# Optimization experiments

Hardware: AMD Instinct MI355X
Metric: run time of the kernel (lower is better)

The kernel has to match this reference:

```python
import jax, jax.numpy as jnp
import numpy as np

LR = 0.01
WD = 0.01


def _lfltm(params, x):
    w1, b1, w2, b2 = params
    return jnp.tanh(x @ w1 + b1) @ w2 + b2  # [N, D]


def _deep_opt_elem(Wm1, bm1, Wm2, bm2, g):
    # per-parameter-element learned optimizer: scalar grad -> hidden(M) -> scalar update
    h = jnp.tanh(g[..., None] * Wm1 + bm1)  # [..., M]
    return h @ Wm2 + bm2[0]


def setup_inputs() -> dict:
    key = jax.random.key(0)
    ks = jax.random.split(key, 8)
    N, D, H, M = 16384, 512, 1024, 32
    return {
        "x_t": jax.random.normal(ks[0], (N, D), jnp.float32),
        "x_target": jax.random.normal(ks[1], (N, D), jnp.float32),
        "w1": jax.random.normal(ks[2], (D, H), jnp.float32) * 0.02,
        "b1": jnp.zeros((H,), jnp.float32),
        "w2": jax.random.normal(ks[3], (H, D), jnp.float32) * 0.02,
        "b2": jnp.zeros((D,), jnp.float32),
        "Wm1": jax.random.normal(ks[4], (M,), jnp.float32) * 0.1,
        "bm1": jnp.zeros((M,), jnp.float32),
        "Wm2": jax.random.normal(ks[5], (M,), jnp.float32) * 0.1,
        "bm2": jnp.zeros((1,), jnp.float32),
    }


def reference(x_t, x_target, w1, b1, w2, b2, Wm1, bm1, Wm2, bm2):
    mem = (w1, b1, w2, b2)

    # retrieve: h_t = LFLTM(memory_state, x_t)
    h_t = _lfltm(mem, x_t)

    # analytic per-step gradient of MSE loss through the memory MLP
    def compute_loss(params):
        pred = _lfltm(params, x_t)
        return jnp.mean((pred - x_target) ** 2)

    grads = jax.grad(compute_loss)(mem)

    # learned optimizer on each gradient tensor, then fast-weight update
    new_mem = tuple(
        p - (LR * _deep_opt_elem(Wm1, bm1, Wm2, bm2, g) + WD * p)
        for p, g in zip(mem, grads)
    )

    return (h_t,) + new_mem
```

## Files before the change

### kernel.cpp

```cpp
#include <hip/hip_runtime.h>
#include <hip/hip_bf16.h>

#define LR 0.01f
#define WD 0.01f
#define NTHREADS 256

typedef short s16x8 __attribute__((ext_vector_type(8)));
typedef float f32x4 __attribute__((ext_vector_type(4)));
typedef unsigned short u16;

__device__ __forceinline__ u16 f2bf(float f) {
    __hip_bfloat16 h = __float2bfloat16(f);
    return *reinterpret_cast<u16*>(&h);
}
__device__ __forceinline__ float bf2f(u16 u) {
    __hip_bfloat16 h;
    *reinterpret_cast<u16*>(&h) = u;
    return __bfloat162float(h);
}
__device__ __forceinline__ float tanh_fast(float x) {
    float t = fminf(fmaxf(2.f * x, -30.f), 30.f);
    float e = __expf(t);
    return 1.f - 2.f * __builtin_amdgcn_rcpf(e + 1.f);
}

__device__ __forceinline__ void stage_pair(const u16* gA, const u16* gB, int ldg,
                                           u16* lds) {
    const int t = threadIdx.x;
#pragma unroll
    for (int q = 0; q < 4; ++q) {
        int s = t + q * 256;
        int row = s >> 3, chp = s & 7;
        int chl = chp ^ (row & 7);
        const u16* gp = (chl < 4) ? (gA + (size_t)row * ldg + chl * 8)
                                  : (gB + (size_t)row * ldg + (chl & 3) * 8);
        __builtin_amdgcn_global_load_lds(
            (const __attribute__((address_space(1))) void*)gp,
            (__attribute__((address_space(3))) void*)(lds + s * 8), 16, 0, 0);
    }
}

__device__ __forceinline__ s16x8 frag(const u16* P, int r, int c) {
    return *(const s16x8*)(P + r * 64 + ((c ^ (r & 7)) * 8));
}

template <int NPROD, int EPI>
__global__ __launch_bounds__(NTHREADS) void k_mfma(
    const u16* __restrict__ Ah, const u16* __restrict__ Al,
    const u16* __restrict__ Bh, const u16* __restrict__ Bl,
    int nbx, int Md, int Nd, int Kd, int Kslice,
    const float* __restrict__ bias, const float* __restrict__ xtgt,
    const u16* __restrict__ Th,
    float* __restrict__ outf, u16* __restrict__ outb, u16* __restrict__ outbT,
    float scale) {
    constexpr int PAIRS = (NPROD > 1) ? 2 : 1;
    __shared__ u16 smem[2 * PAIRS * 8192];

    const int nwg = gridDim.x;
    const int sw = (blockIdx.x & 7) * (nwg >> 3) + (blockIdx.x >> 3);
    const int m0 = (sw / nbx) * 128, n0 = (sw % nbx) * 128;
    const int kb = blockIdx.y * Kslice;

    const int lane = threadIdx.x & 63, wid = threadIdx.x >> 6;
    const int wrow = (wid >> 1) * 64, wcol = (wid & 1) * 64;
    const int lm = lane & 15;
    const int cA = lane >> 4;

    f32x4 acc[4][4] = {};

    const u16* gAh = Ah + (size_t)m0 * Kd + kb;
    const u16* gBh = Bh + (size_t)n0 * Kd + kb;
    const u16* gAl = (NPROD == 3) ? Al + (size_t)m0 * Kd + kb : nullptr;
    const u16* gBl = (NPROD >= 2) ? Bl + (size_t)n0 * Kd + kb : nullptr;

    auto stage_all = [&](int buf, int ko) {
        u16* base = smem + buf * (PAIRS * 8192);
        stage_pair(gAh + ko, gBh + ko, Kd, base);
        if (NPROD == 3) stage_pair(gAl + ko, gBl + ko, Kd, base + 8192);
        if (NPROD == 2) stage_pair(gBl + ko, gBl + ko, Kd, base + 8192);
    };

    stage_all(0, 0);
    __syncthreads();

    int cur = 0;
    for (int k0 = 0; k0 < Kslice; k0 += 32, cur ^= 1) {
        if (k0 + 32 < Kslice) stage_all(cur ^ 1, k0 + 32);
        const u16* P1 = smem + cur * (PAIRS * 8192);
        const u16* P2 = P1 + 8192;
        s16x8 ah[4], bh[4], al[4], bl[4];
#pragma unroll
        for (int i = 0; i < 4; ++i) {
            ah[i] = frag(P1, wrow + i * 16 + lm, cA);
            bh[i] = frag(P1, wcol + i * 16 + lm, cA + 4);
            if (NPROD == 3) {
                al[i] = frag(P2, wrow + i * 16 + lm, cA);
                bl[i] = frag(P2, wcol + i * 16 + lm, cA + 4);
            }
            if (NPROD == 2) bl[i] = frag(P2, wcol + i * 16 + lm, cA);
        }
#pragma unroll
        for (int i = 0; i < 4; ++i)
#pragma unroll
            for (int j = 0; j < 4; ++j) {
                acc[i][j] = __builtin_amdgcn_mfma_f32_16x16x32_bf16(
                    ah[i], bh[j], acc[i][j], 0, 0, 0);
                if (NPROD >= 2)
                    acc[i][j] = __builtin_amdgcn_mfma_f32_16x16x32_bf16(
                        ah[i], bl[j], acc[i][j], 0, 0, 0);
                if (NPROD == 3)
                    acc[i][j] = __builtin_amdgcn_mfma_f32_16x16x32_bf16(
                        al[i], bh[j], acc[i][j], 0, 0, 0);
            }
        __syncthreads();
    }

    const int rbase = (lane >> 4) * 4;
#pragma unroll
    for (int i = 0; i < 4; ++i) {
        const int row0 = m0 + wrow + i * 16 + rbase;
#pragma unroll
        for (int j = 0; j < 4; ++j) {
            const int col = n0 + wcol + j * 16 + lm;
            if (EPI == 0) {
                ushort4 hv;
                float b = bias[col];
                hv.x = f2bf(tanh_fast(acc[i][j][0] + b));
                hv.y = f2bf(tanh_fast(acc[i][j][1] + b));
                hv.z = f2bf(tanh_fast(acc[i][j][2] + b));
                hv.w = f2bf(tanh_fast(acc[i][j][3] + b));
                outb[(size_t)(row0 + 0) * Nd + col] = hv.x;
                outb[(size_t)(row0 + 1) * Nd + col] = hv.y;
                outb[(size_t)(row0 + 2) * Nd + col] = hv.z;
                outb[(size_t)(row0 + 3) * Nd + col] = hv.w;
                *(ushort4*)(outbT + (size_t)col * Md + row0) = hv;
            } else if (EPI == 1) {
                ushort4 gv;
#pragma unroll
                for (int r = 0; r < 4; ++r) {
                    size_t idx = (size_t)(row0 + r) * Nd + col;
                    float p = acc[i][j][r] + bias[col];
                    outf[idx] = p;
                    u16 g = f2bf(scale * (p - xtgt[idx]));
                    outb[idx] = g;
                    ((u16*)&gv)[r] = g;
                }
                *(ushort4*)(outbT + (size_t)col * Md + row0) = gv;
            } else if (EPI == 2) {
                ushort4 dv;
#pragma unroll
                for (int r = 0; r < 4; ++r) {
                    size_t idx = (size_t)(row0 + r) * Nd + col;
                    float tv = bf2f(Th[idx]);
                    ((u16*)&dv)[r] = f2bf(acc[i][j][r] * (1.0f - tv * tv));
                }
                *(ushort4*)(outbT + (size_t)col * Md + row0) = dv;
            } else {
#pragma unroll
                for (int r = 0; r < 4; ++r)
                    atomicAdd(&outf[(size_t)(row0 + r) * Nd + col], acc[i][j][r]);
            }
        }
    }
}

__global__ void k_prep(const float* __restrict__ in, u16* __restrict__ hiRM,
                       u16* __restrict__ loRM, u16* __restrict__ hiT,
                       u16* __restrict__ loT, int R, int C) {
    __shared__ float tile[64][65];
    const int tx = threadIdx.x & 63, ty = threadIdx.x >> 6;
    const int c0 = blockIdx.x * 64, r0 = blockIdx.y * 64;
#pragma unroll
    for (int i = 0; i < 64; i += 4) {
        size_t idx = (size_t)(r0 + ty + i) * C + c0 + tx;
        float v = in[idx];
        tile[ty + i][tx] = v;
        if (hiRM) {
            u16 h = f2bf(v);
            hiRM[idx] = h;
            if (loRM) loRM[idx] = f2bf(v - bf2f(h));
        }
    }
    __syncthreads();
    if (hiT) {
#pragma unroll
        for (int i = 0; i < 64; i += 4) {
            float v = tile[tx][ty + i];
            u16 h = f2bf(v);
            size_t o = (size_t)(c0 + ty + i) * R + r0 + tx;
            hiT[o] = h;
            if (loT) loT[o] = f2bf(v - bf2f(h));
        }
    }
}

__global__ void k_rowsum(const u16* __restrict__ src, float* __restrict__ dst,
                         int C) {
    const int row = blockIdx.x * 4 + (threadIdx.x >> 6);
    const int lane = threadIdx.x & 63;
    const u16* p = src + (size_t)row * C;
    float s = 0.f;
    for (int c = lane * 8; c < C; c += 64 * 8) {
        s16x8 v = *(const s16x8*)(p + c);
#pragma unroll
        for (int e = 0; e < 8; ++e) s += bf2f((u16)v[e]);
    }
#pragma unroll
    for (int off = 32; off; off >>= 1) s += __shfl_down(s, off);
    if (lane == 0) dst[row] = s;
}

__global__ void k_update(const float* __restrict__ p, const float* __restrict__ g,
                         float* __restrict__ out, int n,
                         const float* __restrict__ Wm1, const float* __restrict__ bm1,
                         const float* __restrict__ Wm2, const float* __restrict__ bm2,
                         int M) {
    __shared__ float s1[64], s2[64], s3[64];
    if (threadIdx.x < M) {
        s1[threadIdx.x] = Wm1[threadIdx.x];
        s2[threadIdx.x] = bm1[threadIdx.x];
        s3[threadIdx.x] = Wm2[threadIdx.x];
    }
    __syncthreads();
    int i = blockIdx.x * blockDim.x + threadIdx.x;
    if (i >= n) return;
    float gv = g[i];
    float u = bm2[0];
#pragma unroll 8
    for (int m = 0; m < M; ++m) u += tanh_fast(fmaf(gv, s1[m], s2[m])) * s3[m];
    float pv = p[i];
    out[i] = pv - (LR * u + WD * pv);
}

__global__ void k_zero(float* __restrict__ p, int n) {
    int i = blockIdx.x * blockDim.x + threadIdx.x;
    if (i < n) p[i] = 0.f;
}

extern "C" void kernel_launch(void* const* d_in, const int* in_sizes, int n_in,
                              void* d_out, int out_size, void* d_ws, size_t ws_size,
                              hipStream_t stream) {
    const float* x_t      = (const float*)d_in[0];
    const float* x_target = (const float*)d_in[1];
    const float* w1  = (const float*)d_in[2];
    const float* b1  = (const float*)d_in[3];
    const float* w2  = (const float*)d_in[4];
    const float* b2  = (const float*)d_in[5];
    const float* Wm1 = (const float*)d_in[6];
    const float* bm1 = (const float*)d_in[7];
    const float* Wm2 = (const float*)d_in[8];
    const float* bm2 = (const float*)d_in[9];

    const int H = in_sizes[3];
    const int D = in_sizes[5];
    const int N = in_sizes[0] / D;
    const int M = in_sizes[6];

    char* w = (char*)d_ws;
    float* gw2 = (float*)w;            w += (size_t)H * D * 4;
    float* gw1 = (float*)w;            w += (size_t)D * H * 4;
    float* gb1 = (float*)w;            w += (size_t)H * 4;
    float* gb2 = (float*)w;            w += (size_t)D * 4;
    u16* T_hi = (u16*)w;               w += (size_t)N * H * 2;
    u16* TT   = (u16*)w;               w += (size_t)N * H * 2;
    u16* dAT  = (u16*)w;               w += (size_t)N * H * 2;
    u16* Gb   = (u16*)w;               w += (size_t)N * D * 2;
    u16* x_hi = (u16*)w;               w += (size_t)N * D * 2;
    u16* x_lo = (u16*)w;               w += (size_t)N * D * 2;
    u16* xT   = (u16*)w;               w += (size_t)N * D * 2;
    u16* w1T_hi = (u16*)w;             w += (size_t)D * H * 2;
    u16* w1T_lo = (u16*)w;             w += (size_t)D * H * 2;
    u16* w2T_hi = (u16*)w;             w += (size_t)D * H * 2;
    u16* w2T_lo = (u16*)w;             w += (size_t)D * H * 2;
    u16* w2b_hi = (u16*)w;             w += (size_t)H * D * 2;
    u16* GT = x_lo;

    float* out  = (float*)d_out;
    float* h_t  = out;
    float* o_w1 = h_t + (size_t)N * D;
    float* o_b1 = o_w1 + (size_t)D * H;
    float* o_w2 = o_b1 + H;
    float* o_b2 = o_w2 + (size_t)H * D;

    dim3 blk(NTHREADS);
    const float scale = 2.0f / ((float)N * (float)D);

    int zn = H * D + D * H;
    k_zero<<<dim3((zn + NTHREADS - 1) / NTHREADS), blk, 0, stream>>>(gw2, zn);

    k_prep<<<dim3(D / 64, N / 64), blk, 0, stream>>>(x_t, x_hi, x_lo, xT, nullptr, N, D);
    k_prep<<<dim3(H / 64, D / 64), blk, 0, stream>>>(w1, nullptr, nullptr, w1T_hi, w1T_lo, D, H);
    k_prep<<<dim3(D / 64, H / 64), blk, 0, stream>>>(w2, w2b_hi, nullptr, w2T_hi, w2T_lo, H, D);

    k_mfma<3, 0><<<dim3((H / 128) * (N / 128), 1), blk, 0, stream>>>(
        x_hi, x_lo, w1T_hi, w1T_lo, H / 128, N, H, D, D, b1, nullptr, nullptr,
        nullptr, T_hi, TT, 0.f);

    k_mfma<2, 1><<<dim3((D / 128) * (N / 128), 1), blk, 0, stream>>>(
        T_hi, nullptr, w2T_hi, w2T_lo, D / 128, N, D, H, H, b2, x_target, nullptr,
        h_t, Gb, GT, scale);

    k_mfma<1, 2><<<dim3((H / 128) * (N / 128), 1), blk, 0, stream>>>(
        Gb, nullptr, w2b_hi, nullptr, H / 128, N, H, D, D, nullptr, nullptr, T_hi,
        nullptr, nullptr, dAT, 0.f);

    const int SPLIT = 16;
    k_mfma<1, 3><<<dim3((D / 128) * (H / 128), SPLIT), blk, 0, stream>>>(
        TT, nullptr, GT, nullptr, D / 128, H, D, N, N / SPLIT, nullptr, nullptr,
        nullptr, gw2, nullptr, nullptr, 0.f);

    k_mfma<1, 3><<<dim3((H / 128) * (D / 128), SPLIT), blk, 0, stream>>>(
        xT, nullptr, dAT, nullptr, H / 128, D, H, N, N / SPLIT, nullptr, nullptr,
        nullptr, gw1, nullptr, nullptr, 0.f);

    k_rowsum<<<dim3(H / 4), blk, 0, stream>>>(dAT, gb1, N);
    k_rowsum<<<dim3(D / 4), blk, 0, stream>>>(GT, gb2, N);

    k_update<<<dim3((D * H + NTHREADS - 1) / NTHREADS), blk, 0, stream>>>(
        w1, gw1, o_w1, D * H, Wm1, bm1, Wm2, bm2, M);
    k_update<<<dim3((H + NTHREADS - 1) / NTHREADS), blk, 0, stream>>>(
        b1, gb1, o_b1, H, Wm1, bm1, Wm2, bm2, M);
    k_update<<<dim3((H * D + NTHREADS - 1) / NTHREADS), blk, 0, stream>>>(
        w2, gw2, o_w2, H * D, Wm1, bm1, Wm2, bm2, M);
    k_update<<<dim3((D + NTHREADS - 1) / NTHREADS), blk, 0, stream>>>(
        b2, gb2, o_b2, D, Wm1, bm1, Wm2, bm2, M);
}
```

Before: 440.2 us.

## Replace split-bf16 compensated GEMMs with single fp16 MFMA and scaled gradients

Drops the hi/lo bf16 split products (3 and 2 MFMAs per tile) and runs every GEMM as a single fp16 MFMA pass. To fit the small output gradient in fp16 range, it is pre-scaled by 2^20 and the scale is removed in the update kernel. This cuts the MFMA work, LDS staging and prep traffic for the forward GEMMs. The trade-off is reduced precision (fp16 mantissa, no compensation) and a risk of overflow or underflow in the scaled intermediates.

```diff
diff --git a/kernel.cpp b/kernel.cpp
--- a/kernel.cpp
+++ b/kernel.cpp
@@ -4,19 +4,22 @@
 #define LR 0.01f
 #define WD 0.01f
 #define NTHREADS 256
+#define SCALE_G 1048576.0f
+#define INV_SCALE_G 9.5367431640625e-07f
 
 typedef short s16x8 __attribute__((ext_vector_type(8)));
+typedef _Float16 f16x8 __attribute__((ext_vector_type(8)));
 typedef float f32x4 __attribute__((ext_vector_type(4)));
 typedef unsigned short u16;
 
-__device__ __forceinline__ u16 f2bf(float f) {
-    __hip_bfloat16 h = __float2bfloat16(f);
+__device__ __forceinline__ u16 f2h(float f) {
+    _Float16 h = (_Float16)f;
     return *reinterpret_cast<u16*>(&h);
 }
-__device__ __forceinline__ float bf2f(u16 u) {
-    __hip_bfloat16 h;
+__device__ __forceinline__ float h2f(u16 u) {
+    _Float16 h;
     *reinterpret_cast<u16*>(&h) = u;
-    return __bfloat162float(h);
+    return (float)h;
 }
 __device__ __forceinline__ float tanh_fast(float x) {
     float t = fminf(fmaxf(2.f * x, -30.f), 30.f);
@@ -40,21 +43,19 @@
     }
 }
 
-__device__ __forceinline__ s16x8 frag(const u16* P, int r, int c) {
-    return *(const s16x8*)(P + r * 64 + ((c ^ (r & 7)) * 8));
-}
-
-template <int NPROD, int EPI>
+__device__ __forceinline__ f16x8 frag(const u16* P, int r, int c) {
+    return *(const f16x8*)(P + r * 64 + ((c ^ (r & 7)) * 8));
+}
+
+template <int EPI>
 __global__ __launch_bounds__(NTHREADS) void k_mfma(
-    const u16* __restrict__ Ah, const u16* __restrict__ Al,
-    const u16* __restrict__ Bh, const u16* __restrict__ Bl,
+    const u16* __restrict__ A, const u16* __restrict__ Bt,
     int nbx, int Md, int Nd, int Kd, int Kslice,
     const float* __restrict__ bias, const float* __restrict__ xtgt,
     const u16* __restrict__ Th,
     float* __restrict__ outf, u16* __restrict__ outb, u16* __restrict__ outbT,
     float scale) {
-    constexpr int PAIRS = (NPROD > 1) ? 2 : 1;
-    __shared__ u16 smem[2 * PAIRS * 8192];
+    __shared__ u16 smem[2 * 8192];
 
     const int nwg = gridDim.x;
     const int sw = (blockIdx.x & 7) * (nwg >> 3) + (blockIdx.x >> 3);
@@ -68,50 +69,29 @@
 
     f32x4 acc[4][4] = {};
 
-    const u16* gAh = Ah + (size_t)m0 * Kd + kb;
-    const u16* gBh = Bh + (size_t)n0 * Kd + kb;
-    const u16* gAl = (NPROD == 3) ? Al + (size_t)m0 * Kd + kb : nullptr;
-    const u16* gBl = (NPROD >= 2) ? Bl + (size_t)n0 * Kd + kb : nullptr;
-
-    auto stage_all = [&](int buf, int ko) {
-        u16* base = smem + buf * (PAIRS * 8192);
-        stage_pair(gAh + ko, gBh + ko, Kd, base);
-        if (NPROD == 3) stage_pair(gAl + ko, gBl + ko, Kd, base + 8192);
-        if (NPROD == 2) stage_pair(gBl + ko, gBl + ko, Kd, base + 8192);
-    };
-
-    stage_all(0, 0);
+    const u16* gA = A + (size_t)m0 * Kd + kb;
+    const u16* gB = Bt + (size_t)n0 * Kd + kb;
+
+    stage_pair(gA, gB, Kd, smem);
     __syncthreads();
 
     int cur = 0;
     for (int k0 = 0; k0 < Kslice; k0 += 32, cur ^= 1) {
-        if (k0 + 32 < Kslice) stage_all(cur ^ 1, k0 + 32);
-        const u16* P1 = smem + cur * (PAIRS * 8192);
-        const u16* P2 = P1 + 8192;
-        s16x8 ah[4], bh[4], al[4], bl[4];
+        if (k0 + 32 < Kslice)
+            stage_pair(gA + k0 + 32, gB + k0 + 32, Kd, smem + (cur ^ 1) * 8192);
+        const u16* P1 = smem + cur * 8192;
+        f16x8 a[4], b[4];
 #pragma unroll
         for (int i = 0; i < 4; ++i) {
-            ah[i] = frag(P1, wrow + i * 16 + lm, cA);
-            bh[i] = frag(P1, wcol + i * 16 + lm, cA + 4);
-            if (NPROD == 3) {
-                al[i] = frag(P2, wrow + i * 16 + lm, cA);
-                bl[i] = frag(P2, wcol + i * 16 + lm, cA + 4);
-            }
-            if (NPROD == 2) bl[i] = frag(P2, wcol + i * 16 + lm, cA);
+            a[i] = frag(P1, wrow + i * 16 + lm, cA);
+            b[i] = frag(P1, wcol + i * 16 + lm, cA + 4);
         }
 #pragma unroll
         for (int i = 0; i < 4; ++i)
 #pragma unroll
-            for (int j = 0; j < 4; ++j) {
-                acc[i][j] = __builtin_amdgcn_mfma_f32_16x16x32_bf16(
-                    ah[i], bh[j], acc[i][j], 0, 0, 0);
-                if (NPROD >= 2)
-                    acc[i][j] = __builtin_amdgcn_mfma_f32_16x16x32_bf16(
-                        ah[i], bl[j], acc[i][j], 0, 0, 0);
-                if (NPROD == 3)
-                    acc[i][j] = __builtin_amdgcn_mfma_f32_16x16x32_bf16(
-                        al[i], bh[j], acc[i][j], 0, 0, 0);
-            }
+            for (int j = 0; j < 4; ++j)
+                acc[i][j] = __builtin_amdgcn_mfma_f32_16x16x32_f16(
+                    a[i], b[j], acc[i][j], 0, 0, 0);
         __syncthreads();
     }
 
@@ -124,11 +104,11 @@
             const int col = n0 + wcol + j * 16 + lm;
             if (EPI == 0) {
                 ushort4 hv;
-                float b = bias[col];
-                hv.x = f2bf(tanh_fast(acc[i][j][0] + b));
-                hv.y = f2bf(tanh_fast(acc[i][j][1] + b));
-                hv.z = f2bf(tanh_fast(acc[i][j][2] + b));
-                hv.w = f2bf(tanh_fast(acc[i][j][3] + b));
+                float bcol = bias[col];
+                hv.x = f2h(tanh_fast(acc[i][j][0] + bcol));
+                hv.y = f2h(tanh_fast(acc[i][j][1] + bcol));
+                hv.z = f2h(tanh_fast(acc[i][j][2] + bcol));
+                hv.w = f2h(tanh_fast(acc[i][j][3] + bcol));
                 outb[(size_t)(row0 + 0) * Nd + col] = hv.x;
                 outb[(size_t)(row0 + 1) * Nd + col] = hv.y;
                 outb[(size_t)(row0 + 2) * Nd + col] = hv.z;
@@ -141,7 +121,7 @@
                     size_t idx = (size_t)(row0 + r) * Nd + col;
                     float p = acc[i][j][r] + bias[col];
                     outf[idx] = p;
-                    u16 g = f2bf(scale * (p - xtgt[idx]));
+                    u16 g = f2h(scale * (p - xtgt[idx]));
                     outb[idx] = g;
                     ((u16*)&gv)[r] = g;
                 }
@@ -151,8 +131,8 @@
 #pragma unroll
                 for (int r = 0; r < 4; ++r) {
                     size_t idx = (size_t)(row0 + r) * Nd + col;
-                    float tv = bf2f(Th[idx]);
-                    ((u16*)&dv)[r] = f2bf(acc[i][j][r] * (1.0f - tv * tv));
+                    float tv = h2f(Th[idx]);
+                    ((u16*)&dv)[r] = f2h(acc[i][j][r] * (1.0f - tv * tv));
                 }
                 *(ushort4*)(outbT + (size_t)col * Md + row0) = dv;
             } else {
@@ -164,9 +144,8 @@
     }
 }
 
-__global__ void k_prep(const float* __restrict__ in, u16* __restrict__ hiRM,
-                       u16* __restrict__ loRM, u16* __restrict__ hiT,
-                       u16* __restrict__ loT, int R, int C) {
+__global__ void k_prep(const float* __restrict__ in, u16* __restrict__ rm,
+                       u16* __restrict__ tr, int R, int C) {
     __shared__ float tile[64][65];
     const int tx = threadIdx.x & 63, ty = threadIdx.x >> 6;
     const int c0 = blockIdx.x * 64, r0 = blockIdx.y * 64;
@@ -175,22 +154,13 @@
         size_t idx = (size_t)(r0 + ty + i) * C + c0 + tx;
         float v = in[idx];
         tile[ty + i][tx] = v;
-        if (hiRM) {
-            u16 h = f2bf(v);
-            hiRM[idx] = h;
-            if (loRM) loRM[idx] = f2bf(v - bf2f(h));
-        }
+        if (rm) rm[idx] = f2h(v);
     }
     __syncthreads();
-    if (hiT) {
-#pragma unroll
-        for (int i = 0; i < 64; i += 4) {
-            float v = tile[tx][ty + i];
-            u16 h = f2bf(v);
-            size_t o = (size_t)(c0 + ty + i) * R + r0 + tx;
-            hiT[o] = h;
-            if (loT) loT[o] = f2bf(v - bf2f(h));
-        }
+    if (tr) {
+#pragma unroll
+        for (int i = 0; i < 64; i += 4)
+            tr[(size_t)(c0 + ty + i) * R + r0 + tx] = f2h(tile[tx][ty + i]);
     }
 }
 
@@ -203,7 +173,7 @@
     for (int c = lane * 8; c < C; c += 64 * 8) {
         s16x8 v = *(const s16x8*)(p + c);
 #pragma unroll
-        for (int e = 0; e < 8; ++e) s += bf2f((u16)v[e]);
+        for (int e = 0; e < 8; ++e) s += h2f((u16)v[e]);
     }
 #pragma unroll
     for (int off = 32; off; off >>= 1) s += __shfl_down(s, off);
@@ -214,7 +184,7 @@
                          float* __restrict__ out, int n,
                          const float* __restrict__ Wm1, const float* __restrict__ bm1,
                          const float* __restrict__ Wm2, const float* __restrict__ bm2,
-                         int M) {
+                         int M, float invScale) {
     __shared__ float s1[64], s2[64], s3[64];
     if (threadIdx.x < M) {
         s1[threadIdx.x] = Wm1[threadIdx.x];
@@ -224,7 +194,7 @@
     __syncthreads();
     int i = blockIdx.x * blockDim.x + threadIdx.x;
     if (i >= n) return;
-    float gv = g[i];
+    float gv = g[i] * invScale;
     float u = bm2[0];
 #pragma unroll 8
     for (int m = 0; m < M; ++m) u += tanh_fast(fmaf(gv, s1[m], s2[m])) * s3[m];
@@ -261,19 +231,16 @@
     float* gw1 = (float*)w;            w += (size_t)D * H * 4;
     float* gb1 = (float*)w;            w += (size_t)H * 4;
     float* gb2 = (float*)w;            w += (size_t)D * 4;
-    u16* T_hi = (u16*)w;               w += (size_t)N * H * 2;
+    u16* Tf   = (u16*)w;               w += (size_t)N * H * 2;
     u16* TT   = (u16*)w;               w += (size_t)N * H * 2;
     u16* dAT  = (u16*)w;               w += (size_t)N * H * 2;
     u16* Gb   = (u16*)w;               w += (size_t)N * D * 2;
-    u16* x_hi = (u16*)w;               w += (size_t)N * D * 2;
-    u16* x_lo = (u16*)w;               w += (size_t)N * D * 2;
+    u16* GT   = (u16*)w;               w += (size_t)N * D * 2;
+    u16* xf   = (u16*)w;               w += (size_t)N * D * 2;
     u16* xT   = (u16*)w;               w += (size_t)N * D * 2;
-    u16* w1T_hi = (u16*)w;             w += (size_t)D * H * 2;
-    u16* w1T_lo = (u16*)w;             w += (size_t)D * H * 2;
-    u16* w2T_hi = (u16*)w;             w += (size_t)D * H * 2;
-    u16* w2T_lo = (u16*)w;             w += (size_t)D * H * 2;
-    u16* w2b_hi = (u16*)w;             w += (size_t)H * D * 2;
-    u16* GT = x_lo;
+    u16* w1T  = (u16*)w;               w += (size_t)D * H * 2;
+    u16* w2T  = (u16*)w;               w += (size_t)D * H * 2;
+    u16* w2b  = (u16*)w;               w += (size_t)H * D * 2;
 
     float* out  = (float*)d_out;
     float* h_t  = out;
@@ -283,45 +250,45 @@
     float* o_b2 = o_w2 + (size_t)H * D;
 
     dim3 blk(NTHREADS);
-    const float scale = 2.0f / ((float)N * (float)D);
+    const float scaleG = (2.0f / ((float)N * (float)D)) * SCALE_G;
 
     int zn = H * D + D * H;
     k_zero<<<dim3((zn + NTHREADS - 1) / NTHREADS), blk, 0, stream>>>(gw2, zn);
 
-    k_prep<<<dim3(D / 64, N / 64), blk, 0, stream>>>(x_t, x_hi, x_lo, xT, nullptr, N, D);
-    k_prep<<<dim3(H / 64, D / 64), blk, 0, stream>>>(w1, nullptr, nullptr, w1T_hi, w1T_lo, D, H);
-    k_prep<<<dim3(D / 64, H / 64), blk, 0, stream>>>(w2, w2b_hi, nullptr, w2T_hi, w2T_lo, H, D);
-
-    k_mfma<3, 0><<<dim3((H / 128) * (N / 128), 1), blk, 0, stream>>>(
-        x_hi, x_lo, w1T_hi, w1T_lo, H / 128, N, H, D, D, b1, nullptr, nullptr,
-        nullptr, T_hi, TT, 0.f);
-
-    k_mfma<2, 1><<<dim3((D / 128) * (N / 128), 1), blk, 0, stream>>>(
-        T_hi, nullptr, w2T_hi, w2T_lo, D / 128, N, D, H, H, b2, x_target, nullptr,
-        h_t, Gb, GT, scale);
-
-    k_mfma<1, 2><<<dim3((H / 128) * (N / 128), 1), blk, 0, stream>>>(
-        Gb, nullptr, w2b_hi, nullptr, H / 128, N, H, D, D, nullptr, nullptr, T_hi,
+    k_prep<<<dim3(D / 64, N / 64), blk, 0, stream>>>(x_t, xf, xT, N, D);
+    k_prep<<<dim3(H / 64, D / 64), blk, 0, stream>>>(w1, nullptr, w1T, D, H);
+    k_prep<<<dim3(D / 64, H / 64), blk, 0, stream>>>(w2, w2b, w2T, H, D);
+
+    k_mfma<0><<<dim3((H / 128) * (N / 128), 1), blk, 0, stream>>>(
+        xf, w1T, H / 128, N, H, D, D, b1, nullptr, nullptr,
+        nullptr, Tf, TT, 0.f);
+
+    k_mfma<1><<<dim3((D / 128) * (N / 128), 1), blk, 0, stream>>>(
+        Tf, w2T, D / 128, N, D, H, H, b2, x_target, nullptr,
+        h_t, Gb, GT, scaleG);
+
+    k_mfma<2><<<dim3((H / 128) * (N / 128), 1), blk, 0, stream>>>(
+        Gb, w2b, H / 128, N, H, D, D, nullptr, nullptr, Tf,
         nullptr, nullptr, dAT, 0.f);
 
     const int SPLIT = 16;
-    k_mfma<1, 3><<<dim3((D / 128) * (H / 128), SPLIT), blk, 0, stream>>>(
-        TT, nullptr, GT, nullptr, D / 128, H, D, N, N / SPLIT, nullptr, nullptr,
-        nullptr, gw2, nullptr, nullptr, 0.f);
-
-    k_mfma<1, 3><<<dim3((H / 128) * (D / 128), SPLIT), blk, 0, stream>>>(
-        xT, nullptr, dAT, nullptr, H / 128, D, H, N, N / SPLIT, nullptr, nullptr,
-        nullptr, gw1, nullptr, nullptr, 0.f);
+    k_mfma<3><<<dim3((D / 128) * (H / 128), SPLIT), blk, 0, stream>>>(
+        TT, GT, D / 128, H, D, N, N / SPLIT, nullptr, nullptr, nullptr,
+        gw2, nullptr, nullptr, 0.f);
+
+    k_mfma<3><<<dim3((H / 128) * (D / 128), SPLIT), blk, 0, stream>>>(
+        xT, dAT, H / 128, D, H, N, N / SPLIT, nullptr, nullptr, nullptr,
+        gw1, nullptr, nullptr, 0.f);
 
     k_rowsum<<<dim3(H / 4), blk, 0, stream>>>(dAT, gb1, N);
     k_rowsum<<<dim3(D / 4), blk, 0, stream>>>(GT, gb2, N);
 
     k_update<<<dim3((D * H + NTHREADS - 1) / NTHREADS), blk, 0, stream>>>(
-        w1, gw1, o_w1, D * H, Wm1, bm1, Wm2, bm2, M);
+        w1, gw1, o_w1, D * H, Wm1, bm1, Wm2, bm2, M, INV_SCALE_G);
     k_update<<<dim3((H + NTHREADS - 1) / NTHREADS), blk, 0, stream>>>(
-        b1, gb1, o_b1, H, Wm1, bm1, Wm2, bm2, M);
+        b1, gb1, o_b1, H, Wm1, bm1, Wm2, bm2, M, INV_SCALE_G);
     k_update<<<dim3((H * D + NTHREADS - 1) / NTHREADS), blk, 0, stream>>>(
-        w2, gw2, o_w2, H * D, Wm1, bm1, Wm2, bm2, M);
+        w2, gw2, o_w2, H * D, Wm1, bm1, Wm2, bm2, M, INV_SCALE_G);
     k_update<<<dim3((D + NTHREADS - 1) / NTHREADS), blk, 0, stream>>>(
-        b2, gb2, o_b2, D, Wm1, bm1, Wm2, bm2, M);
-}
+        b2, gb2, o_b2, D, Wm1, bm1, Wm2, bm2, M, INV_SCALE_G);
+}
```

After: 422.0 us. 4.1% less time.
